# Kernel optimization log

Hardware: AMD Instinct MI355X
Metric: run time of the kernel (lower is better)

## Reference

```python
import jax, jax.numpy as jnp
import numpy as np

WINDOW_SIZE = 11
SIGMA = 1.5
C1 = 0.01 ** 2
C2 = 0.03 ** 2


def _make_window(channel, dtype=jnp.float32):
    # Faithful to torch `gaussian`: center at window_size/2 (= 5.5 for ws=11)
    x = np.arange(WINDOW_SIZE, dtype=np.float64)
    g = np.exp(-((x - WINDOW_SIZE / 2) ** 2) / (2.0 * SIGMA ** 2))
    g = (g / g.sum()).astype(np.float32)
    w2d = np.outer(g, g)  # (ws, ws)
    w = np.broadcast_to(w2d, (channel, 1, WINDOW_SIZE, WINDOW_SIZE)).copy()
    return jnp.asarray(w, dtype=dtype)


def _dwconv(x, w, channel):
    pad = WINDOW_SIZE // 2
    return jax.lax.conv_general_dilated(
        x, w,
        window_strides=(1, 1),
        padding=[(pad, pad), (pad, pad)],
        dimension_numbers=("NCHW", "OIHW", "NCHW"),
        feature_group_count=channel,
    )


def setup_inputs() -> dict:
    key = jax.random.key(0)
    k1, k2 = jax.random.split(key)
    B, C, H, W = 16, 3, 512, 512
    img1 = jax.random.uniform(k1, (B, C, H, W), dtype=jnp.float32)
    img2 = jax.random.uniform(k2, (B, C, H, W), dtype=jnp.float32)
    return {"img1": img1, "img2": img2}


def reference(img1, img2):
    channel = img1.shape[1]
    window = _make_window(channel, img1.dtype)

    mu1 = _dwconv(img1, window, channel)
    mu2 = _dwconv(img2, window, channel)
    mu1_sq = mu1 * mu1
    mu2_sq = mu2 * mu2
    mu1_mu2 = mu1 * mu2

    sigma1_sq = _dwconv(img1 * img1, window, channel) - mu1_sq
    sigma2_sq = _dwconv(img2 * img2, window, channel) - mu2_sq
    sigma12 = _dwconv(img1 * img2, window, channel) - mu1_mu2

    numerator = (2 * mu1_mu2 + C1) * (2 * sigma12 + C2)
    denominator = (mu1_sq + mu2_sq + C1) * (sigma1_sq + sigma2_sq + C2)
    ssim_map = numerator / denominator
    return jnp.mean(ssim_map)  # size_average=True
```

## Files before the change

kernel.cpp:

```cpp
#include <hip/hip_runtime.h>
#include <cmath>


#define IMG_H 512
#define IMG_W 512
#define STRIPE 32
#define NSTR (IMG_H / STRIPE)
#define NPLANES 48
#define NBLOCKS (NPLANES * NSTR)
#define SSIM_C1 (0.01f * 0.01f)
#define SSIM_C2 (0.03f * 0.03f)

struct W11 { float w[11]; };

__attribute__((amdgpu_flat_work_group_size(512, 512), amdgpu_waves_per_eu(1, 2)))
__global__ void ssim_main(const float* __restrict__ img1,
                          const float* __restrict__ img2,
                          float* __restrict__ blockSums, W11 wv) {
    __shared__ float2 tb[2][528];
    __shared__ float red[8];

    const int x = threadIdx.x;
    const int bid = blockIdx.x;
    const int plane = bid >> 4;
    const int stripe = bid & (NSTR - 1);
    const int y0 = stripe * STRIPE;
    const size_t base = (size_t)plane * (IMG_H * IMG_W);

    if (x < 10) {
        const int col = (x < 5) ? x : (x + 512);
        tb[0][col] = make_float2(0.f, 0.f);
        tb[1][col] = make_float2(0.f, 0.f);
    }

    float rA[11], rB[11], rS[11], rP[11];
    float acc = 0.f;

    float pa = 0.f, pb = 0.f;
    {
        const int r0 = y0 - 5;
        if (r0 >= 0) {
            pa = img1[base + (size_t)r0 * IMG_W + x];
            pb = img2[base + (size_t)r0 * IMG_W + x];
        }
    }

    int buf = 0;
#pragma unroll 1
    for (int c = 0; c < 4; ++c) {
#pragma unroll
        for (int j = 0; j < 11; ++j) {
            const int i = c * 11 + j;
            if (i < 42) {
                tb[buf][x + 5] = make_float2(pa, pb);
                pa = 0.f; pb = 0.f;
                const int rn = y0 - 4 + i;
                if (i + 1 < 42 && rn >= 0 && rn < IMG_H) {
                    pa = img1[base + (size_t)rn * IMG_W + x];
                    pb = img2[base + (size_t)rn * IMG_W + x];
                }
                __syncthreads();
                float h0 = 0.f, h1 = 0.f, h2 = 0.f, h3 = 0.f;
#pragma unroll
                for (int k = 0; k < 11; ++k) {
                    const float2 t = tb[buf][x + k];
                    const float w = wv.w[k];
                    const float sq = fmaf(t.y, t.y, t.x * t.x);
                    const float pr = t.x * t.y;
                    h0 = fmaf(w, t.x, h0);
                    h1 = fmaf(w, t.y, h1);
                    h2 = fmaf(w, sq, h2);
                    h3 = fmaf(w, pr, h3);
                }
                rA[j] = h0; rB[j] = h1; rS[j] = h2; rP[j] = h3;

                if (i >= 10) {
                    float vA = 0.f, vB = 0.f, vS = 0.f, vP = 0.f;
#pragma unroll
                    for (int k = 0; k < 11; ++k) {
                        const int s = (j + 1 + k) % 11;
                        const float w = wv.w[k];
                        vA = fmaf(w, rA[s], vA);
                        vB = fmaf(w, rB[s], vB);
                        vS = fmaf(w, rS[s], vS);
                        vP = fmaf(w, rP[s], vP);
                    }
                    const float mu11 = vA * vA;
                    const float mu22 = vB * vB;
                    const float mu12 = vA * vB;
                    const float num = fmaf(2.f, mu12, SSIM_C1) *
                                      fmaf(2.f, vP - mu12, SSIM_C2);
                    const float d1  = mu11 + mu22;
                    const float den = (d1 + SSIM_C1) * ((vS - d1) + SSIM_C2);
                    acc = fmaf(num, __builtin_amdgcn_rcpf(den), acc);
                }
                buf ^= 1;
            }
        }
    }

#pragma unroll
    for (int off = 32; off >= 1; off >>= 1)
        acc += __shfl_down(acc, off, 64);
    const int wave = x >> 6, lane = x & 63;
    if (lane == 0) red[wave] = acc;
    __syncthreads();
    if (x == 0) {
        float s = 0.f;
#pragma unroll
        for (int k = 0; k < 8; ++k) s += red[k];
        blockSums[bid] = s;
    }
}

__global__ void ssim_reduce(const float* __restrict__ bs,
                            float* __restrict__ out) {
    __shared__ double red[4];
    const int t = threadIdx.x;
    double a = 0.0;
    for (int idx = t; idx < NBLOCKS; idx += 256) a += (double)bs[idx];
#pragma unroll
    for (int off = 32; off >= 1; off >>= 1)
        a += __shfl_down(a, off, 64);
    const int wave = t >> 6, lane = t & 63;
    if (lane == 0) red[wave] = a;
    __syncthreads();
    if (t == 0) {
        const double s = red[0] + red[1] + red[2] + red[3];
        out[0] = (float)(s / (double)((double)NPLANES * IMG_H * IMG_W));
    }
}

extern "C" void kernel_launch(void* const* d_in, const int* in_sizes, int n_in,
                              void* d_out, int out_size, void* d_ws, size_t ws_size,
                              hipStream_t stream) {
    const float* img1 = (const float*)d_in[0];
    const float* img2 = (const float*)d_in[1];
    float* out = (float*)d_out;
    float* bs = (float*)d_ws;

    W11 wv;
    double g[11], s = 0.0;
    for (int i = 0; i < 11; ++i) {
        const double d = (double)i - 5.5;
        g[i] = exp(-(d * d) / (2.0 * 1.5 * 1.5));
        s += g[i];
    }
    for (int i = 0; i < 11; ++i) wv.w[i] = (float)(g[i] / s);

    ssim_main<<<NBLOCKS, 512, 0, stream>>>(img1, img2, bs, wv);
    ssim_reduce<<<1, 256, 0, stream>>>(bs, out);
}
```

Baseline: 151.6 us.

## Make each wave own a private 64-column strip with halo loads, removing block barriers

Each wave now handles its own 64-column slice of a 32-row stripe and keeps a private LDS row buffer. The 10 halo columns are loaded by extra lanes, so no __syncthreads is needed per row; only compiler memory fences remain. The centre tap is computed from registers, the next row's load is issued after the row is staged, and blocks shrink to 256 threads with per-wave partial sums reduced by a 1024-thread final kernel. The intent is to remove block-wide barrier stalls, at the cost of redundant halo global loads and a single-buffered LDS that relies on wave-level lockstep execution.

```diff
diff --git a/kernel.cpp b/kernel.cpp
--- a/kernel.cpp
+++ b/kernel.cpp
@@ -5,129 +5,150 @@
 #define IMG_H 512
 #define IMG_W 512
 #define STRIPE 32
-#define NSTR (IMG_H / STRIPE)
+#define NSTR 16
 #define NPLANES 48
-#define NBLOCKS (NPLANES * NSTR)
+#define NWAVES (NPLANES * NSTR * 8)
+#define NBLOCKS (NWAVES / 4)
 #define SSIM_C1 (0.01f * 0.01f)
 #define SSIM_C2 (0.03f * 0.03f)
 
+#define WAVE_MEM_FENCE() asm volatile("" ::: "memory")
+
 struct W11 { float w[11]; };
 
-__attribute__((amdgpu_flat_work_group_size(512, 512), amdgpu_waves_per_eu(1, 2)))
+__attribute__((amdgpu_flat_work_group_size(256, 256), amdgpu_waves_per_eu(1)))
 __global__ void ssim_main(const float* __restrict__ img1,
                           const float* __restrict__ img2,
-                          float* __restrict__ blockSums, W11 wv) {
-    __shared__ float2 tb[2][528];
-    __shared__ float red[8];
+                          float* __restrict__ waveSums, W11 wv) {
+    __shared__ float2 tb[4][80];
 
-    const int x = threadIdx.x;
+    const int tid = threadIdx.x;
+    const int wia = tid >> 6;
+    const int l   = tid & 63;
     const int bid = blockIdx.x;
-    const int plane = bid >> 4;
-    const int stripe = bid & (NSTR - 1);
+    const int plane  = bid >> 5;
+    const int rem    = bid & 31;
+    const int stripe = rem >> 1;
+    const int half   = rem & 1;
+    const int c0 = half * 256 + wia * 64;
     const int y0 = stripe * STRIPE;
-    const size_t base = (size_t)plane * (IMG_H * IMG_W);
+    const int col = c0 + l;
 
-    if (x < 10) {
-        const int col = (x < 5) ? x : (x + 512);
-        tb[0][col] = make_float2(0.f, 0.f);
-        tb[1][col] = make_float2(0.f, 0.f);
-    }
+    const float* __restrict__ p1 = img1 + (size_t)plane * (IMG_H * IMG_W);
+    const float* __restrict__ p2 = img2 + (size_t)plane * (IMG_H * IMG_W);
+
+    float2* buf = tb[wia];
+
+    const bool hlane  = (l < 10);
+    const int  hraw   = (l < 5) ? (c0 - 5 + l) : (c0 + 59 + l);
+    const bool hvalid = hlane && (hraw >= 0) && (hraw < IMG_W);
+    const int  hcol   = hvalid ? hraw : 0;
+    const int  hslot  = (l < 5) ? l : (l + 64);
 
     float rA[11], rB[11], rS[11], rP[11];
     float acc = 0.f;
+    float pa = 0.f, pb = 0.f, hpa = 0.f, hpb = 0.f;
 
-    float pa = 0.f, pb = 0.f;
-    {
-        const int r0 = y0 - 5;
-        if (r0 >= 0) {
-            pa = img1[base + (size_t)r0 * IMG_W + x];
-            pb = img2[base + (size_t)r0 * IMG_W + x];
-        }
+#define LOAD_ROW(RI) do {                                                   \
+    const int ri_ = (RI);                                                   \
+    if (ri_ >= 0 && ri_ < IMG_H) {                 \
+        const size_t off_ = (size_t)ri_ * IMG_W;                            \
+        pa = p1[off_ + col]; pb = p2[off_ + col];                           \
+        if (hlane) {                                                        \
+            const float ta_ = p1[off_ + hcol], tb_ = p2[off_ + hcol];       \
+            hpa = hvalid ? ta_ : 0.f; hpb = hvalid ? tb_ : 0.f;             \
+        }                                                                   \
+    } else { pa = 0.f; pb = 0.f; hpa = 0.f; hpb = 0.f; }                    \
+} while (0)
+
+#define STAGE_AND_H(PHASE, RINEXT) do {                                     \
+    WAVE_MEM_FENCE();                                                       \
+    buf[l + 5] = make_float2(pa, pb);                                       \
+    if (hlane) buf[hslot] = make_float2(hpa, hpb);                          \
+    WAVE_MEM_FENCE();                                                       \
+    float h0_, h1_, h2_, h3_;                                               \
+    { const float w_ = wv.w[5];                                             \
+      const float sq_ = fmaf(pb, pb, pa * pa);                              \
+      const float pr_ = pa * pb;                                            \
+      h0_ = w_ * pa; h1_ = w_ * pb; h2_ = w_ * sq_; h3_ = w_ * pr_; }       \
+    LOAD_ROW(RINEXT);                                                       \
+    _Pragma("unroll")                                                       \
+    for (int k_ = 0; k_ < 11; ++k_) {                                       \
+        if (k_ != 5) {                                                      \
+            const float2 t_ = buf[l + k_];                 \
+            const float w_ = wv.w[k_];                                      \
+            const float sq_ = fmaf(t_.y, t_.y, t_.x * t_.x);                \
+            const float pr_ = t_.x * t_.y;                                  \
+            h0_ = fmaf(w_, t_.x, h0_); h1_ = fmaf(w_, t_.y, h1_);           \
+            h2_ = fmaf(w_, sq_, h2_);  h3_ = fmaf(w_, pr_, h3_);            \
+        }                                                                   \
+    }                                                                       \
+    rA[PHASE] = h0_; rB[PHASE] = h1_;                                       \
+    rS[PHASE] = h2_; rP[PHASE] = h3_;                                       \
+} while (0)
+
+    LOAD_ROW(y0 - 5);
+
+#pragma unroll
+    for (int i = 0; i < 10; ++i) {
+        STAGE_AND_H(i, y0 - 4 + i);
     }
 
-    int buf = 0;
 #pragma unroll 1
-    for (int c = 0; c < 4; ++c) {
+    for (int outer = 0; outer < 3; ++outer) {
 #pragma unroll
-        for (int j = 0; j < 11; ++j) {
-            const int i = c * 11 + j;
-            if (i < 42) {
-                tb[buf][x + 5] = make_float2(pa, pb);
-                pa = 0.f; pb = 0.f;
-                const int rn = y0 - 4 + i;
-                if (i + 1 < 42 && rn >= 0 && rn < IMG_H) {
-                    pa = img1[base + (size_t)rn * IMG_W + x];
-                    pb = img2[base + (size_t)rn * IMG_W + x];
-                }
-                __syncthreads();
-                float h0 = 0.f, h1 = 0.f, h2 = 0.f, h3 = 0.f;
+        for (int jj = 0; jj < 11; ++jj) {
+            const int m = outer * 11 + jj;
+            if (m < 32) {
+                STAGE_AND_H((10 + jj) % 11, (m < 31) ? (y0 + 6 + m) : -1);
+                float vA = 0.f, vB = 0.f, vS = 0.f, vP = 0.f;
 #pragma unroll
                 for (int k = 0; k < 11; ++k) {
-                    const float2 t = tb[buf][x + k];
+                    const int s = (jj + k) % 11;
                     const float w = wv.w[k];
-                    const float sq = fmaf(t.y, t.y, t.x * t.x);
-                    const float pr = t.x * t.y;
-                    h0 = fmaf(w, t.x, h0);
-                    h1 = fmaf(w, t.y, h1);
-                    h2 = fmaf(w, sq, h2);
-                    h3 = fmaf(w, pr, h3);
+                    vA = fmaf(w, rA[s], vA);
+                    vB = fmaf(w, rB[s], vB);
+                    vS = fmaf(w, rS[s], vS);
+                    vP = fmaf(w, rP[s], vP);
                 }
-                rA[j] = h0; rB[j] = h1; rS[j] = h2; rP[j] = h3;
-
-                if (i >= 10) {
-                    float vA = 0.f, vB = 0.f, vS = 0.f, vP = 0.f;
-#pragma unroll
-                    for (int k = 0; k < 11; ++k) {
-                        const int s = (j + 1 + k) % 11;
-                        const float w = wv.w[k];
-                        vA = fmaf(w, rA[s], vA);
-                        vB = fmaf(w, rB[s], vB);
-                        vS = fmaf(w, rS[s], vS);
-                        vP = fmaf(w, rP[s], vP);
-                    }
-                    const float mu11 = vA * vA;
-                    const float mu22 = vB * vB;
-                    const float mu12 = vA * vB;
-                    const float num = fmaf(2.f, mu12, SSIM_C1) *
-                                      fmaf(2.f, vP - mu12, SSIM_C2);
-                    const float d1  = mu11 + mu22;
-                    const float den = (d1 + SSIM_C1) * ((vS - d1) + SSIM_C2);
-                    acc = fmaf(num, __builtin_amdgcn_rcpf(den), acc);
-                }
-                buf ^= 1;
+                const float mu11 = vA * vA;
+                const float mu22 = vB * vB;
+                const float mu12 = vA * vB;
+                const float num = fmaf(2.f, mu12, SSIM_C1) *
+                                  fmaf(2.f, vP - mu12, SSIM_C2);
+                const float d1  = mu11 + mu22;
+                const float den = (d1 + SSIM_C1) * ((vS - d1) + SSIM_C2);
+                acc = fmaf(num, __builtin_amdgcn_rcpf(den), acc);
             }
         }
     }
 
+#undef LOAD_ROW
+#undef STAGE_AND_H
+
 #pragma unroll
     for (int off = 32; off >= 1; off >>= 1)
         acc += __shfl_down(acc, off, 64);
-    const int wave = x >> 6, lane = x & 63;
-    if (lane == 0) red[wave] = acc;
-    __syncthreads();
-    if (x == 0) {
-        float s = 0.f;
-#pragma unroll
-        for (int k = 0; k < 8; ++k) s += red[k];
-        blockSums[bid] = s;
-    }
+    if (l == 0) waveSums[bid * 4 + wia] = acc;
 }
 
-__global__ void ssim_reduce(const float* __restrict__ bs,
+__global__ void ssim_reduce(const float* __restrict__ ws,
                             float* __restrict__ out) {
-    __shared__ double red[4];
+    __shared__ double red[16];
     const int t = threadIdx.x;
     double a = 0.0;
-    for (int idx = t; idx < NBLOCKS; idx += 256) a += (double)bs[idx];
+    for (int i = t; i < NWAVES; i += 1024) a += (double)ws[i];
 #pragma unroll
     for (int off = 32; off >= 1; off >>= 1)
         a += __shfl_down(a, off, 64);
-    const int wave = t >> 6, lane = t & 63;
-    if (lane == 0) red[wave] = a;
+    const int wv_ = t >> 6, lane = t & 63;
+    if (lane == 0) red[wv_] = a;
     __syncthreads();
     if (t == 0) {
-        const double s = red[0] + red[1] + red[2] + red[3];
-        out[0] = (float)(s / (double)((double)NPLANES * IMG_H * IMG_W));
+        double s = 0.0;
+#pragma unroll
+        for (int k = 0; k < 16; ++k) s += red[k];
+        out[0] = (float)(s / ((double)NPLANES * IMG_H * IMG_W));
     }
 }
 
@@ -137,7 +158,7 @@
     const float* img1 = (const float*)d_in[0];
     const float* img2 = (const float*)d_in[1];
     float* out = (float*)d_out;
-    float* bs = (float*)d_ws;
+    float* wsums = (float*)d_ws;
 
     W11 wv;
     double g[11], s = 0.0;
@@ -148,6 +169,6 @@
     }
     for (int i = 0; i < 11; ++i) wv.w[i] = (float)(g[i] / s);
 
-    ssim_main<<<NBLOCKS, 512, 0, stream>>>(img1, img2, bs, wv);
-    ssim_reduce<<<1, 256, 0, stream>>>(bs, out);
+    ssim_main<<<NBLOCKS, 256, 0, stream>>>(img1, img2, wsums, wv);
+    ssim_reduce<<<1, 1024, 0, stream>>>(wsums, out);
 }
```

After: 284.9 us. 87.9% more time.
